# Kernel optimization log

Hardware: AMD Instinct MI355X
Metric: run time of the kernel (lower is better)

## Reference

```python
import jax, jax.numpy as jnp
import numpy as np

B, C, H, W = 32, 16, 256, 256
NUM_BINS = 9
LEVELS = 3
EPS = 1e-8

def _dw_kernels():
    lap = np.array([[0, 1, 0], [1, -4, 1], [0, 1, 0]], np.float32)
    sx = np.array([[-1, 0, 1], [-2, 0, 2], [-1, 0, 1]], np.float32)
    sy = np.array([[-1, -2, -1], [0, 0, 0], [1, 2, 1]], np.float32)
    rep = lambda k: np.tile(k[None, None], (C, 1, 1, 1))  # [C,1,3,3] depthwise
    return rep(lap), rep(sx), rep(sy)

def setup_inputs() -> dict:
    key = jax.random.key(0)
    x = jax.random.normal(key, (B, C, H, W), dtype=jnp.float32)
    lap_k, sx_k, sy_k = _dw_kernels()
    return {"x": x, "lap_k": jnp.asarray(lap_k), "sx_k": jnp.asarray(sx_k), "sy_k": jnp.asarray(sy_k)}

def _dwconv(x, k):
    # depthwise 3x3, padding=1, groups=C
    return jax.lax.conv_general_dilated(
        x, k, window_strides=(1, 1), padding=[(1, 1), (1, 1)],
        dimension_numbers=("NCHW", "OIHW", "NCHW"), feature_group_count=C)

def reference(x, lap_k, sx_k, sy_k):
    lap = _dwconv(x, lap_k)
    gx = _dwconv(lap, sx_k)
    gy = _dwconv(lap, sy_k)
    mag = jnp.sqrt(gx * gx + gy * gy + EPS)
    ang = jnp.mod(jnp.arctan2(gy, gx) * (180.0 / np.pi), 180.0)
    bin_size = 180.0 / NUM_BINS
    bins = jnp.floor((ang + 0.5 * bin_size) / bin_size).astype(jnp.int32) % NUM_BINS

    BC = B * C
    mag_bc = mag.reshape(BC, H * W)
    bins_bc = bins.reshape(BC, H * W)
    row_ids = jnp.arange(BC)[:, None]

    hists = []
    for lvl in range(LEVELS):
        cs = 2 ** lvl
        cell_h, cell_w = H // cs, W // cs
        Wc = W // cell_w
        rows = jnp.arange(H) // cell_h
        cols = jnp.arange(W) // cell_w
        cell_id = (rows[:, None] * Wc + cols[None, :]).reshape(-1)  # [H*W]
        num_cells = cs * cs
        idx = cell_id[None, :] * NUM_BINS + bins_bc  # [BC, H*W]
        hist = jnp.zeros((BC, num_cells * NUM_BINS), mag.dtype).at[row_ids, idx].add(mag_bc)
        hist = hist.reshape(BC, num_cells, NUM_BINS)
        hist = hist / (hist.sum(axis=-1, keepdims=True) + EPS)          # L1-ish norm
        norm = jnp.sqrt(jnp.sum(hist * hist, axis=-1, keepdims=True))
        hist = hist / jnp.maximum(norm, 1e-12)                          # F.normalize p=2
        hists.append(hist.reshape(B, C * num_cells, NUM_BINS))
    out = jnp.concatenate(hists, axis=1)[:, None]  # [B,1,C*(1+4+16),num_bins]
    return out
```

## Files before the change

kernel.cpp:

```cpp
#include <hip/hip_runtime.h>


#define H_IMG 256
#define W_IMG 256

#define BS0 1.7364817766693033e34f
#define BC0 9.84807753012208e34f
#define BS1 5.0e34f
#define BC1 8.660254037844387e34f
#define BS2 7.66044443118978e34f
#define BC2 6.427876096865393e34f
#define BS3 9.396926207859084e34f
#define BC3 3.420201433256687e34f

__device__ __forceinline__ void lap_row6(float dst[6], const float u[8], const float m[8],
                                         const float d[8], float wm0, float wm5) {
#pragma unroll
  for (int c = 0; c < 6; ++c)
    dst[c] = (u[c + 1] + d[c + 1]) + fmaf(-4.f, m[c + 1], m[c] + m[c + 2]);
  dst[0] *= wm0;
  dst[5] *= wm5;
}

__device__ __forceinline__ void lap_row6_rm(float dst[6], const float u[8], const float m[8],
                                            const float d[8], float wm0, float wm5, float rowm) {
#pragma unroll
  for (int c = 0; c < 6; ++c) {
    float v = (u[c + 1] + d[c + 1]) + fmaf(-4.f, m[c + 1], m[c] + m[c + 2]);
    dst[c] = v * rowm;
  }
  dst[0] *= wm0;
  dst[5] *= wm5;
}

__device__ __forceinline__ void out_row4(const float A[6], const float B[6], const float C[6],
                                         float acc[10]) {
  float cs[6], dd[6];
#pragma unroll
  for (int c = 0; c < 6; ++c) {
    cs[c] = A[c] + fmaf(2.f, B[c], C[c]);
    dd[c] = C[c] - A[c];
  }
#pragma unroll
  for (int c = 0; c < 4; ++c) {
    float gx = cs[c + 2] - cs[c];
    float gy = fmaf(2.f, dd[c + 1], dd[c] + dd[c + 2]);
    float mag = __builtin_amdgcn_sqrtf(fmaf(gx, gx, fmaf(gy, gy, 1e-8f)));
    unsigned sg = __float_as_uint(gy) & 0x80000000u;
    float fx = __uint_as_float(__float_as_uint(gx) ^ sg);
    float fy = fabsf(gy);
    float b0 = fx * BS0;
    float b1 = fx * BS1;
    float b2 = fx * BS2;
    float b3 = fx * BS3;
    acc[0] = fmaf(mag, __builtin_amdgcn_fmed3f(fmaf(fy, BC0, -b0), 0.f, 1.f), acc[0]);
    acc[1] = fmaf(mag, __builtin_amdgcn_fmed3f(fmaf(fy, BC1, -b1), 0.f, 1.f), acc[1]);
    acc[2] = fmaf(mag, __builtin_amdgcn_fmed3f(fmaf(fy, BC2, -b2), 0.f, 1.f), acc[2]);
    acc[3] = fmaf(mag, __builtin_amdgcn_fmed3f(fmaf(fy, BC3, -b3), 0.f, 1.f), acc[3]);
    acc[4] = fmaf(mag, __builtin_amdgcn_fmed3f(fx * -1e35f, 0.f, 1.f), acc[4]);
    acc[5] = fmaf(mag, __builtin_amdgcn_fmed3f(fmaf(fy, -BC3, -b3), 0.f, 1.f), acc[5]);
    acc[6] = fmaf(mag, __builtin_amdgcn_fmed3f(fmaf(fy, -BC2, -b2), 0.f, 1.f), acc[6]);
    acc[7] = fmaf(mag, __builtin_amdgcn_fmed3f(fmaf(fy, -BC1, -b1), 0.f, 1.f), acc[7]);
    acc[8] = fmaf(mag, __builtin_amdgcn_fmed3f(fmaf(fy, -BC0, -b0), 0.f, 1.f), acc[8]);
    acc[9] += mag;
  }
}

__device__ __forceinline__ void load_grow(const float* __restrict__ xim, int gr, bool valid,
                                          int o0, int o1, int o2, int o3,
                                          float mlo, float mhi, float r[8]) {
  if (valid) {
    const float* p = xim + gr * W_IMG;
    float2 a = *reinterpret_cast<const float2*>(p + o0);
    float2 b = *reinterpret_cast<const float2*>(p + o1);
    float2 c = *reinterpret_cast<const float2*>(p + o2);
    float2 d = *reinterpret_cast<const float2*>(p + o3);
    r[0] = a.x * mlo; r[1] = a.y * mlo;
    r[2] = b.x;       r[3] = b.y;
    r[4] = c.x;       r[5] = c.y;
    r[6] = d.x * mhi; r[7] = d.y * mhi;
  } else {
#pragma unroll
    for (int i = 0; i < 8; ++i) r[i] = 0.f;
  }
}

__global__ __launch_bounds__(256) void phog_hist_kernel(const float* __restrict__ x,
                                                        float* __restrict__ hist2) {
  const int f = blockIdx.y * 8 + blockIdx.x;
  const int xcd = f & 7;
  const int idx = f >> 3;
  const int bc = xcd * 64 + (idx >> 3);
  const int half = idx & 7;
  const int tr2 = half >> 2;
  const int tc = half & 3;
  const int R0 = tr2 * 128;
  const int C0 = tc * 64;
  const int tid = threadIdx.x;
  const int tcol = tid & 15;
  const int trow = tid >> 4;

  const float* xim = x + (size_t)bc * (H_IMG * W_IMG);

  const int gr0 = R0 + 8 * trow;
  const int gc0 = C0 + 4 * tcol;
  const int bcol = gc0 - 2;

  const int o0 = (bcol < 0) ? 0 : bcol;
  const int o1 = gc0;
  const int o2 = gc0 + 2;
  const int o3 = (gc0 + 4 > 254) ? 254 : (gc0 + 4);
  const float mlo = (bcol >= 0) ? 1.f : 0.f;
  const float mhi = (gc0 + 5 <= 255) ? 1.f : 0.f;

  const bool vlo = gr0 > 0;
  const bool vhi = gr0 < 248;
  const float rm_first = vlo ? 1.f : 0.f;
  const float rm_last = vhi ? 1.f : 0.f;
  const float wm0 = (gc0 >= 1) ? 1.f : 0.f;
  const float wm5 = (gc0 + 4 <= 255) ? 1.f : 0.f;

  float w0[8], w1[8], w2[8], w3[8], w4[8], w5[8];
  float w6[8], w7[8], w8[8], w9[8], w10[8], w11[8];
  load_grow(xim, gr0 - 2, vlo, o0, o1, o2, o3, mlo, mhi, w0);
  load_grow(xim, gr0 - 1, vlo, o0, o1, o2, o3, mlo, mhi, w1);
  load_grow(xim, gr0 + 0, true, o0, o1, o2, o3, mlo, mhi, w2);
  load_grow(xim, gr0 + 1, true, o0, o1, o2, o3, mlo, mhi, w3);
  load_grow(xim, gr0 + 2, true, o0, o1, o2, o3, mlo, mhi, w4);
  load_grow(xim, gr0 + 3, true, o0, o1, o2, o3, mlo, mhi, w5);
  load_grow(xim, gr0 + 4, true, o0, o1, o2, o3, mlo, mhi, w6);
  load_grow(xim, gr0 + 5, true, o0, o1, o2, o3, mlo, mhi, w7);
  load_grow(xim, gr0 + 6, true, o0, o1, o2, o3, mlo, mhi, w8);
  load_grow(xim, gr0 + 7, true, o0, o1, o2, o3, mlo, mhi, w9);
  load_grow(xim, gr0 + 8, vhi, o0, o1, o2, o3, mlo, mhi, w10);
  load_grow(xim, gr0 + 9, vhi, o0, o1, o2, o3, mlo, mhi, w11);

  float acc[10];
#pragma unroll
  for (int k = 0; k < 10; ++k) acc[k] = 0.f;

  float lA[6], lB[6], lC[6], lD[6];
  lap_row6_rm(lA, w0, w1, w2, wm0, wm5, rm_first);
  lap_row6(lB, w1, w2, w3, wm0, wm5);
  lap_row6(lC, w2, w3, w4, wm0, wm5);
  out_row4(lA, lB, lC, acc);
  lap_row6(lD, w3, w4, w5, wm0, wm5);
  out_row4(lB, lC, lD, acc);
  lap_row6(lA, w4, w5, w6, wm0, wm5);
  out_row4(lC, lD, lA, acc);
  lap_row6(lB, w5, w6, w7, wm0, wm5);
  out_row4(lD, lA, lB, acc);
  lap_row6(lC, w6, w7, w8, wm0, wm5);
  out_row4(lA, lB, lC, acc);
  lap_row6(lD, w7, w8, w9, wm0, wm5);
  out_row4(lB, lC, lD, acc);
  lap_row6(lA, w8, w9, w10, wm0, wm5);
  out_row4(lC, lD, lA, acc);
  lap_row6_rm(lB, w9, w10, w11, wm0, wm5, rm_last);
  out_row4(lD, lA, lB, acc);

#pragma unroll
  for (int k = 0; k < 10; ++k) {
    float v = acc[k];
#pragma unroll
    for (int off = 32; off > 0; off >>= 1) v += __shfl_xor(v, off);
    acc[k] = v;
  }

  __shared__ float hred[4][10];
  __shared__ float hs[2][10];
  const int lane = tid & 63;
  const int wave = tid >> 6;
  if (lane == 0) {
#pragma unroll
    for (int k = 0; k < 10; ++k) hred[wave][k] = acc[k];
  }
  __syncthreads();
  if (tid < 10) hs[0][tid] = hred[0][tid] + hred[1][tid];
  if (tid >= 32 && tid < 42) hs[1][tid - 32] = hred[2][tid - 32] + hred[3][tid - 32];
  __syncthreads();

  const int cell_top = (2 * tr2) * 4 + tc;
  const int cell_bot = (2 * tr2 + 1) * 4 + tc;
  if (tid < 9) {
    float h = (tid == 0) ? ((hs[0][9] - hs[0][0]) + hs[0][8]) : (hs[0][tid - 1] - hs[0][tid]);
    hist2[(bc * 16 + cell_top) * 9 + tid] = h;
  }
  if (tid >= 32 && tid < 41) {
    int k = tid - 32;
    float h = (k == 0) ? ((hs[1][9] - hs[1][0]) + hs[1][8]) : (hs[1][k - 1] - hs[1][k]);
    hist2[(bc * 16 + cell_bot) * 9 + k] = h;
  }
}

__global__ __launch_bounds__(256) void phog_norm_kernel(const float* __restrict__ hist2,
                                                        float* __restrict__ out) {
  int t = blockIdx.x * 256 + threadIdx.x;
  if (t >= 32 * 336) return;
  int b = t / 336;
  int r = t - b * 336;

  float h[9];
  if (r < 16) {
    const float* p = hist2 + (b * 16 + r) * 144;
#pragma unroll
    for (int k = 0; k < 9; ++k) {
      float s = 0.f;
#pragma unroll
      for (int cell = 0; cell < 16; ++cell) s += p[cell * 9 + k];
      h[k] = s;
    }
  } else if (r < 80) {
    int q = r - 16;
    int c = q >> 2;
    int cell = q & 3;
    int r1 = cell >> 1, c1 = cell & 1;
    const float* p = hist2 + (b * 16 + c) * 144;
    int i00 = ((2 * r1) * 4 + 2 * c1) * 9;
    int i01 = ((2 * r1) * 4 + 2 * c1 + 1) * 9;
    int i10 = ((2 * r1 + 1) * 4 + 2 * c1) * 9;
    int i11 = ((2 * r1 + 1) * 4 + 2 * c1 + 1) * 9;
#pragma unroll
    for (int k = 0; k < 9; ++k) h[k] = (p[i00 + k] + p[i01 + k]) + (p[i10 + k] + p[i11 + k]);
  } else {
    int q = r - 80;
    int c = q >> 4;
    int cell = q & 15;
    const float* p = hist2 + ((b * 16 + c) * 16 + cell) * 9;
#pragma unroll
    for (int k = 0; k < 9; ++k) h[k] = p[k];
  }

  float s = 0.f;
#pragma unroll
  for (int k = 0; k < 9; ++k) s += h[k];
  float inv = 1.f / (s + 1e-8f);
#pragma unroll
  for (int k = 0; k < 9; ++k) h[k] *= inv;
  float n2 = 0.f;
#pragma unroll
  for (int k = 0; k < 9; ++k) n2 = fmaf(h[k], h[k], n2);
  float nrm = sqrtf(n2);
  float inv2 = 1.f / fmaxf(nrm, 1e-12f);
#pragma unroll
  for (int k = 0; k < 9; ++k) out[t * 9 + k] = h[k] * inv2;
}

extern "C" void kernel_launch(void* const* d_in, const int* in_sizes, int n_in,
                              void* d_out, int out_size, void* d_ws, size_t ws_size,
                              hipStream_t stream) {
  const float* x = (const float*)d_in[0];
  float* out = (float*)d_out;
  float* hist2 = (float*)d_ws;

  dim3 g1(8, 512);
  phog_hist_kernel<<<g1, 256, 0, stream>>>(x, hist2);

  int total = 32 * 336;
  phog_norm_kernel<<<(total + 255) / 256, 256, 0, stream>>>(hist2, out);
}
```

Before: 52.86 us.

## Process 16 rows per thread so each wave owns one cell, dropping shared reduction

```diff
diff --git a/kernel.cpp b/kernel.cpp
--- a/kernel.cpp
+++ b/kernel.cpp
@@ -87,22 +87,19 @@
 
 __global__ __launch_bounds__(256) void phog_hist_kernel(const float* __restrict__ x,
                                                         float* __restrict__ hist2) {
-  const int f = blockIdx.y * 8 + blockIdx.x;
+  const int f = blockIdx.y * 4 + blockIdx.x;
   const int xcd = f & 7;
   const int idx = f >> 3;
-  const int bc = xcd * 64 + (idx >> 3);
-  const int half = idx & 7;
-  const int tr2 = half >> 2;
-  const int tc = half & 3;
-  const int R0 = tr2 * 128;
-  const int C0 = tc * 64;
+  const int bc = xcd * 64 + (idx >> 2);
+  const int strip = idx & 3;
+  const int C0 = strip * 64;
   const int tid = threadIdx.x;
   const int tcol = tid & 15;
   const int trow = tid >> 4;
 
   const float* xim = x + (size_t)bc * (H_IMG * W_IMG);
 
-  const int gr0 = R0 + 8 * trow;
+  const int gr0 = 16 * trow;
   const int gc0 = C0 + 4 * tcol;
   const int bcol = gc0 - 2;
 
@@ -113,15 +110,15 @@
   const float mlo = (bcol >= 0) ? 1.f : 0.f;
   const float mhi = (gc0 + 5 <= 255) ? 1.f : 0.f;
 
-  const bool vlo = gr0 > 0;
-  const bool vhi = gr0 < 248;
+  const bool vlo = trow > 0;
+  const bool vhi = trow < 15;
   const float rm_first = vlo ? 1.f : 0.f;
   const float rm_last = vhi ? 1.f : 0.f;
   const float wm0 = (gc0 >= 1) ? 1.f : 0.f;
   const float wm5 = (gc0 + 4 <= 255) ? 1.f : 0.f;
 
-  float w0[8], w1[8], w2[8], w3[8], w4[8], w5[8];
-  float w6[8], w7[8], w8[8], w9[8], w10[8], w11[8];
+  float w0[8], w1[8], w2[8], w3[8], w4[8], w5[8], w6[8], w7[8], w8[8], w9[8];
+  float w10[8], w11[8], w12[8], w13[8], w14[8], w15[8], w16[8], w17[8], w18[8], w19[8];
   load_grow(xim, gr0 - 2, vlo, o0, o1, o2, o3, mlo, mhi, w0);
   load_grow(xim, gr0 - 1, vlo, o0, o1, o2, o3, mlo, mhi, w1);
   load_grow(xim, gr0 + 0, true, o0, o1, o2, o3, mlo, mhi, w2);
@@ -132,8 +129,16 @@
   load_grow(xim, gr0 + 5, true, o0, o1, o2, o3, mlo, mhi, w7);
   load_grow(xim, gr0 + 6, true, o0, o1, o2, o3, mlo, mhi, w8);
   load_grow(xim, gr0 + 7, true, o0, o1, o2, o3, mlo, mhi, w9);
-  load_grow(xim, gr0 + 8, vhi, o0, o1, o2, o3, mlo, mhi, w10);
-  load_grow(xim, gr0 + 9, vhi, o0, o1, o2, o3, mlo, mhi, w11);
+  load_grow(xim, gr0 + 8, true, o0, o1, o2, o3, mlo, mhi, w10);
+  load_grow(xim, gr0 + 9, true, o0, o1, o2, o3, mlo, mhi, w11);
+  load_grow(xim, gr0 + 10, true, o0, o1, o2, o3, mlo, mhi, w12);
+  load_grow(xim, gr0 + 11, true, o0, o1, o2, o3, mlo, mhi, w13);
+  load_grow(xim, gr0 + 12, true, o0, o1, o2, o3, mlo, mhi, w14);
+  load_grow(xim, gr0 + 13, true, o0, o1, o2, o3, mlo, mhi, w15);
+  load_grow(xim, gr0 + 14, true, o0, o1, o2, o3, mlo, mhi, w16);
+  load_grow(xim, gr0 + 15, true, o0, o1, o2, o3, mlo, mhi, w17);
+  load_grow(xim, gr0 + 16, vhi, o0, o1, o2, o3, mlo, mhi, w18);
+  load_grow(xim, gr0 + 17, vhi, o0, o1, o2, o3, mlo, mhi, w19);
 
   float acc[10];
 #pragma unroll
@@ -156,7 +161,23 @@
   out_row4(lB, lC, lD, acc);
   lap_row6(lA, w8, w9, w10, wm0, wm5);
   out_row4(lC, lD, lA, acc);
-  lap_row6_rm(lB, w9, w10, w11, wm0, wm5, rm_last);
+  lap_row6(lB, w9, w10, w11, wm0, wm5);
+  out_row4(lD, lA, lB, acc);
+  lap_row6(lC, w10, w11, w12, wm0, wm5);
+  out_row4(lA, lB, lC, acc);
+  lap_row6(lD, w11, w12, w13, wm0, wm5);
+  out_row4(lB, lC, lD, acc);
+  lap_row6(lA, w12, w13, w14, wm0, wm5);
+  out_row4(lC, lD, lA, acc);
+  lap_row6(lB, w13, w14, w15, wm0, wm5);
+  out_row4(lD, lA, lB, acc);
+  lap_row6(lC, w14, w15, w16, wm0, wm5);
+  out_row4(lA, lB, lC, acc);
+  lap_row6(lD, w15, w16, w17, wm0, wm5);
+  out_row4(lB, lC, lD, acc);
+  lap_row6(lA, w16, w17, w18, wm0, wm5);
+  out_row4(lC, lD, lA, acc);
+  lap_row6_rm(lB, w17, w18, w19, wm0, wm5, rm_last);
   out_row4(lD, lA, lB, acc);
 
 #pragma unroll
@@ -166,30 +187,13 @@
     for (int off = 32; off > 0; off >>= 1) v += __shfl_xor(v, off);
     acc[k] = v;
   }
-
-  __shared__ float hred[4][10];
-  __shared__ float hs[2][10];
   const int lane = tid & 63;
-  const int wave = tid >> 6;
+  const int w = tid >> 6;
   if (lane == 0) {
-#pragma unroll
-    for (int k = 0; k < 10; ++k) hred[wave][k] = acc[k];
-  }
-  __syncthreads();
-  if (tid < 10) hs[0][tid] = hred[0][tid] + hred[1][tid];
-  if (tid >= 32 && tid < 42) hs[1][tid - 32] = hred[2][tid - 32] + hred[3][tid - 32];
-  __syncthreads();
-
-  const int cell_top = (2 * tr2) * 4 + tc;
-  const int cell_bot = (2 * tr2 + 1) * 4 + tc;
-  if (tid < 9) {
-    float h = (tid == 0) ? ((hs[0][9] - hs[0][0]) + hs[0][8]) : (hs[0][tid - 1] - hs[0][tid]);
-    hist2[(bc * 16 + cell_top) * 9 + tid] = h;
-  }
-  if (tid >= 32 && tid < 41) {
-    int k = tid - 32;
-    float h = (k == 0) ? ((hs[1][9] - hs[1][0]) + hs[1][8]) : (hs[1][k - 1] - hs[1][k]);
-    hist2[(bc * 16 + cell_bot) * 9 + k] = h;
+    float* dst = &hist2[((bc * 16) + (w * 4 + strip)) * 9];
+    dst[0] = (acc[9] - acc[0]) + acc[8];
+#pragma unroll
+    for (int k = 1; k < 9; ++k) dst[k] = acc[k - 1] - acc[k];
   }
 }
 
@@ -253,7 +257,7 @@
   float* out = (float*)d_out;
   float* hist2 = (float*)d_ws;
 
-  dim3 g1(8, 512);
+  dim3 g1(4, 512);
   phog_hist_kernel<<<g1, 256, 0, stream>>>(x, hist2);
 
   int total = 32 * 336;
```

Measured after the change: 55.24 us. 1.05x slower.
